# Performance work log

Hardware: AMD Instinct MI355X
Metric: run time of the kernel (lower is better)

The kernel has to match this reference:

```python
import jax, jax.numpy as jnp
import numpy as np

N, N_E, E_DIM = 32768, 4096, 256


def setup_inputs() -> dict:
    key = jax.random.key(0)
    k1, k2 = jax.random.split(key)
    z = jax.random.normal(k1, (N, E_DIM), dtype=jnp.float32)
    # embedding.weight.data.uniform_(-1/n_e, 1/n_e)
    emb = jax.random.uniform(k2, (N_E, E_DIM), dtype=jnp.float32,
                             minval=-1.0 / N_E, maxval=1.0 / N_E)
    return {"z": z, "emb": emb}


def reference(z, emb):
    # pairwise squared L2: ||z||^2 + ||e||^2 - 2 z e^T  -> [N, n_e]
    d = (jnp.sum(z ** 2, axis=1, keepdims=True)
         + jnp.sum(emb ** 2, axis=1)
         - 2.0 * jnp.matmul(z, emb.T))
    min_encoding_indices = jnp.argmin(d, axis=1)              # [N]
    # original builds one-hot scatter and returns it
    min_encodings = jax.nn.one_hot(min_encoding_indices, emb.shape[0],
                                   dtype=z.dtype)             # [N, n_e]
    # one_hot @ emb == direct gather (same math, efficient form)
    z_q = emb[min_encoding_indices]                           # [N, e_dim]
    # loss = mean((z_q - z.detach())^2): codebook loss only (beta unused)
    loss = jnp.mean((z_q - jax.lax.stop_gradient(z)) ** 2)
    # straight-through estimator
    z_q_st = z + jax.lax.stop_gradient(z_q - z)
    return (loss, min_encodings, z_q_st, emb, min_encoding_indices[:, None])
```

## Files before the change

### kernel.cpp

```cpp
#include <hip/hip_runtime.h>
#include <stdint.h>

#define N_ROWS 32768
#define N_E    4096
#define E_DIM  256

typedef __attribute__((ext_vector_type(8))) short short8;
typedef __attribute__((ext_vector_type(4))) float f32x4;

#define GLOAD_LDS16(g, l)                                                     \
    __builtin_amdgcn_global_load_lds(                                         \
        (const __attribute__((address_space(1))) void*)(g),                   \
        (__attribute__((address_space(3))) void*)(l), 16, 0, 0)

__device__ __forceinline__ unsigned int f2sort(float s) {
    unsigned int b = __float_as_uint(s);
    return (b & 0x80000000u) ? ~b : (b | 0x80000000u);
}
__device__ __forceinline__ float sort2f(unsigned int u) {
    unsigned int b = (u & 0x80000000u) ? (u ^ 0x80000000u) : ~u;
    return __uint_as_float(b);
}
__device__ __forceinline__ unsigned short bfr(float x) {
    unsigned int u = __float_as_uint(x);
    return (unsigned short)((u + 0x7fffu + ((u >> 16) & 1u)) >> 16);
}
__device__ __forceinline__ float bf2f(unsigned short h) {
    return __uint_as_float((unsigned int)h << 16);
}

__global__ __launch_bounds__(256) void k_rownorm(const float* __restrict__ src,
                                                 float* __restrict__ outf) {
    int j = blockIdx.x * 4 + (threadIdx.x >> 6);
    int lane = threadIdx.x & 63;
    const float4* e4 = (const float4*)(src + (size_t)j * E_DIM);
    float4 v = e4[lane];
    double s = (double)v.x * v.x + (double)v.y * v.y + (double)v.z * v.z + (double)v.w * v.w;
    #pragma unroll
    for (int off = 1; off < 64; off <<= 1) s += __shfl_xor(s, off);
    if (lane == 0) outf[j] = (float)s;
}

__global__ __launch_bounds__(256) void k_split(const float* __restrict__ src,
                                               unsigned short* __restrict__ hi,
                                               unsigned short* __restrict__ lo) {
    int c = blockIdx.x * 256 + threadIdx.x;
    int r   = c >> 5;
    int kc8 = c & 31;
    const float* p = src + (size_t)c * 8;
    float v[8];
    *(float4*)&v[0] = *(const float4*)p;
    *(float4*)&v[4] = *(const float4*)(p + 4);
    short8 h8, l8;
    #pragma unroll
    for (int t = 0; t < 8; t++) {
        unsigned short h = bfr(v[t]);
        h8[t] = (short)h;
        l8[t] = (short)bfr(v[t] - bf2f(h));
    }
    int kt = kc8 >> 2, lg = kc8 & 3;
    size_t o8 = (size_t)(r >> 4) * 512 + kt * 64 + lg * 16 + (r & 15);
    *(short8*)(hi + o8 * 8) = h8;
    *(short8*)(lo + o8 * 8) = l8;
}

__global__ __launch_bounds__(256, 1) void k_screen(
        const float* __restrict__ z,
        const unsigned short* __restrict__ ehi, const unsigned short* __restrict__ elo,
        const float* __restrict__ enf, const float* __restrict__ znf,
        int* __restrict__ idx, int* __restrict__ flaglist, int* __restrict__ flagcnt,
        float* __restrict__ out) {
    __shared__ short8 BT[8192];

    const int tid  = threadIdx.x;
    const int lane = tid & 63;
    const int w    = tid >> 6;
    const int l15  = lane & 15;
    const int lg   = lane >> 4;
    const int fb0  = blockIdx.x * 8 + w * 2;

    const short8* Gh = (const short8*)ehi;
    const short8* Gl = (const short8*)elo;
    float* zfill = out + (size_t)blockIdx.x * 524288;

    short8 ah[2][8], al[2][8];
    #pragma unroll
    for (int mi = 0; mi < 2; mi++) {
        int row = (fb0 + mi) * 16 + l15;
        const float* zr = z + (size_t)row * E_DIM + lg * 8;
        #pragma unroll
        for (int kt = 0; kt < 8; kt++) {
            float4 v0 = *(const float4*)(zr + kt * 32);
            float4 v1 = *(const float4*)(zr + kt * 32 + 4);
            float v[8] = {v0.x, v0.y, v0.z, v0.w, v1.x, v1.y, v1.z, v1.w};
            short8 h8, l8;
            #pragma unroll
            for (int t = 0; t < 8; t++) {
                unsigned short h = bfr(v[t]);
                h8[t] = (short)h;
                l8[t] = (short)bfr(v[t] - bf2f(h));
            }
            ah[mi][kt] = h8;
            al[mi][kt] = l8;
        }
    }

    float czs[8];
    #pragma unroll
    for (int mi = 0; mi < 2; mi++)
        #pragma unroll
        for (int qi = 0; qi < 4; qi++)
            czs[mi * 4 + qi] = znf[(fb0 + mi) * 16 + lg * 4 + qi];

    unsigned long long K1[8];
    float Qf[8];
    #pragma unroll
    for (int s = 0; s < 8; s++) { K1[s] = ~0ull; Qf[s] = __uint_as_float(0x7F800000u); }

    auto stage = [&](int t, int b) {
        const short8* sh = Gh + (size_t)t * 2048;
        const short8* sl = Gl + (size_t)t * 2048;
        short8* dh = &BT[b * 4096];
        short8* dl = &BT[b * 4096 + 2048];
        #pragma unroll
        for (int i = 0; i < 8; i++) {
            int c = (w * 8 + i) * 64;
            GLOAD_LDS16(sh + c + lane, dh + c);
            GLOAD_LDS16(sl + c + lane, dl + c);
        }
    };

#define LOADB(BH, BL, KT)                                                     \
    _Pragma("unroll")                                                         \
    for (int p = 0; p < 4; p++) {                                             \
        BH[p] = Bc_h[p * 512 + (KT) * 64 + lane];                             \
        BL[p] = Bc_l[p * 512 + (KT) * 64 + lane];                             \
    }
#define DOMFMA(BH, BL, KT)                                                    \
    _Pragma("unroll")                                                         \
    for (int p = 0; p < 4; p++) {                                             \
        _Pragma("unroll")                                                     \
        for (int mi = 0; mi < 2; mi++) {                                      \
            acc[mi][p] = __builtin_amdgcn_mfma_f32_16x16x32_bf16(ah[mi][KT], BH[p], acc[mi][p], 0, 0, 0); \
            acc[mi][p] = __builtin_amdgcn_mfma_f32_16x16x32_bf16(al[mi][KT], BH[p], acc[mi][p], 0, 0, 0); \
            acc[mi][p] = __builtin_amdgcn_mfma_f32_16x16x32_bf16(ah[mi][KT], BL[p], acc[mi][p], 0, 0, 0); \
        }                                                                     \
    }

    int cur = 0;
    stage(0, 0);
    for (int t = 0; t < 64; ++t) {
        __syncthreads();
        if (t + 1 < 64) stage(t + 1, cur ^ 1);

        {
            f32x4 zv4 = {0.f, 0.f, 0.f, 0.f};
            float* dst = zfill + (size_t)t * 8192 + tid * 4;
            #pragma unroll
            for (int i = 0; i < 8; i++)
                __builtin_nontemporal_store(zv4, (f32x4*)(dst + i * 1024));
        }

        const short8* Bc_h = &BT[cur * 4096];
        const short8* Bc_l = &BT[cur * 4096 + 2048];

        f32x4 acc[2][4];
        #pragma unroll
        for (int mi = 0; mi < 2; mi++)
            #pragma unroll
            for (int p = 0; p < 4; p++)
                acc[mi][p] = (f32x4){0.f, 0.f, 0.f, 0.f};

        short8 bhA[4], blA[4], bhB[4], blB[4];
        LOADB(bhA, blA, 0)
        LOADB(bhB, blB, 1)
        DOMFMA(bhA, blA, 0) LOADB(bhA, blA, 2)
        DOMFMA(bhB, blB, 1) LOADB(bhB, blB, 3)
        DOMFMA(bhA, blA, 2) LOADB(bhA, blA, 4)
        DOMFMA(bhB, blB, 3) LOADB(bhB, blB, 5)
        DOMFMA(bhA, blA, 4) LOADB(bhA, blA, 6)
        DOMFMA(bhB, blB, 5) LOADB(bhB, blB, 7)
        DOMFMA(bhA, blA, 6)
        DOMFMA(bhB, blB, 7)

        #pragma unroll
        for (int p = 0; p < 4; p++) {
            int j = t * 64 + p * 16 + l15;
            float Ce = enf[j];
            #pragma unroll
            for (int mi = 0; mi < 2; mi++) {
                #pragma unroll
                for (int qi = 0; qi < 4; qi++) {
                    int s = mi * 4 + qi;
                    float av = acc[mi][p][qi];
                    float A  = czs[s] + Ce;
                    float qv = fmaf(-2.0f, av, A);
                    unsigned long long kk =
                        ((unsigned long long)f2sort(qv) << 32) | (unsigned int)j;
                    if (kk < K1[s]) K1[s] = kk;
                    float res = (A - qv) - 2.0f * av;
                    float u = __uint_as_float(__float_as_uint(qv) & 0x7F800000u)
                              * 1.1920929e-7f;
                    if (fabsf(res) > fmaf(0.5f, u, -1.5e-7f))
                        Qf[s] = fminf(Qf[s], qv);
                }
            }
        }
        cur ^= 1;
    }
#undef LOADB
#undef DOMFMA

    #pragma unroll
    for (int s = 0; s < 8; s++) {
        unsigned long long K = K1[s];
        float Q = Qf[s];
        #pragma unroll
        for (int off = 1; off < 16; off <<= 1) {
            unsigned long long ok = __shfl_xor(K, off);
            float oq = __shfl_xor(Q, off);
            if (ok < K) K = ok;
            Q = fminf(Q, oq);
        }
        if (l15 == 0) {
            int row = blockIdx.x * 128 + w * 32 + (s >> 2) * 16 + lg * 4 + (s & 3);
            idx[row] = (int)(K & 0xFFFFFFFFull);
            float qwin = sort2f((unsigned int)(K >> 32));
            float u = __uint_as_float(__float_as_uint(qwin) & 0x7F800000u) * 1.1920929e-7f;
            if (Q <= fmaf(2.0f, u, qwin)) {
                int pp = atomicAdd(flagcnt, 1);
                flaglist[pp] = row;
            }
        }
    }
}

__global__ __launch_bounds__(256) void k_repair(const float* __restrict__ z,
                                                const float* __restrict__ emb,
                                                const float* __restrict__ enf,
                                                const float* __restrict__ znf,
                                                const int* __restrict__ flagcnt,
                                                const int* __restrict__ flaglist,
                                                unsigned long long* __restrict__ kpart) {
    __shared__ float zr[8][E_DIM];
    __shared__ unsigned long long redk[4][8];
    const int tid = threadIdx.x;
    const int cnt = flagcnt[0];
    const int oct = blockIdx.x >> 2;
    const int qd  = blockIdx.x & 3;

    for (int base = oct * 8; base < cnt; base += 2048) {
        __syncthreads();
        int gr[8];
        #pragma unroll
        for (int r = 0; r < 8; r++) {
            int fi = base + r;
            gr[r] = flaglist[fi < cnt ? fi : base];
        }
        for (int i = tid; i < 8 * 64; i += 256) {
            int r = i >> 6, c4 = i & 63;
            *(float4*)&zr[r][c4 * 4] = *(const float4*)(z + (size_t)gr[r] * E_DIM + c4 * 4);
        }
        __syncthreads();

        float Cz[8];
        #pragma unroll
        for (int r = 0; r < 8; r++) Cz[r] = znf[gr[r]];

        unsigned long long bk[8];
        #pragma unroll
        for (int r = 0; r < 8; r++) bk[r] = ~0ull;

        #pragma unroll
        for (int g = 0; g < 2; g++) {
            const int j0 = qd * 1024 + g * 512 + tid;
            const float* e0 = emb + (size_t)(j0      ) * E_DIM;
            const float* e1 = emb + (size_t)(j0 + 256) * E_DIM;
            float a[8][2];
            #pragma unroll
            for (int r = 0; r < 8; r++) { a[r][0] = 0.0f; a[r][1] = 0.0f; }

            #pragma unroll 4
            for (int k4 = 0; k4 < 64; k4++) {
                float4 v0 = *(const float4*)(e0 + k4 * 4);
                float4 v1 = *(const float4*)(e1 + k4 * 4);
                #pragma unroll
                for (int r = 0; r < 8; r++) {
                    float4 zq = *(const float4*)&zr[r][k4 * 4];
                    a[r][0] = fmaf(zq.x, v0.x, a[r][0]); a[r][0] = fmaf(zq.y, v0.y, a[r][0]);
                    a[r][0] = fmaf(zq.z, v0.z, a[r][0]); a[r][0] = fmaf(zq.w, v0.w, a[r][0]);
                    a[r][1] = fmaf(zq.x, v1.x, a[r][1]); a[r][1] = fmaf(zq.y, v1.y, a[r][1]);
                    a[r][1] = fmaf(zq.z, v1.z, a[r][1]); a[r][1] = fmaf(zq.w, v1.w, a[r][1]);
                }
            }
            float en0 = enf[j0], en1 = enf[j0 + 256];
            #pragma unroll
            for (int r = 0; r < 8; r++) {
                float q0 = (Cz[r] + en0) - 2.0f * a[r][0];
                float q1 = (Cz[r] + en1) - 2.0f * a[r][1];
                unsigned long long k;
                k = ((unsigned long long)f2sort(q0) << 32) | (unsigned int)(j0      ); if (k < bk[r]) bk[r] = k;
                k = ((unsigned long long)f2sort(q1) << 32) | (unsigned int)(j0 + 256); if (k < bk[r]) bk[r] = k;
            }
        }

        const int w = tid >> 6;
        #pragma unroll
        for (int r = 0; r < 8; r++) {
            unsigned long long K = bk[r];
            #pragma unroll
            for (int off = 1; off < 64; off <<= 1) {
                unsigned long long ok = __shfl_xor(K, off);
                if (ok < K) K = ok;
            }
            if ((tid & 63) == 0) redk[w][r] = K;
        }
        __syncthreads();
        if (tid < 8 && base + tid < cnt) {
            unsigned long long K = redk[0][tid];
            #pragma unroll
            for (int wv = 1; wv < 4; wv++)
                if (redk[wv][tid] < K) K = redk[wv][tid];
            kpart[(size_t)(base + tid) * 4 + qd] = K;
        }
    }
}

__global__ __launch_bounds__(256) void k_fin(const int* __restrict__ flagcnt,
                                             const int* __restrict__ flaglist,
                                             const unsigned long long* __restrict__ kpart,
                                             int* __restrict__ idx) {
    const int cnt = flagcnt[0];
    for (int fi = blockIdx.x * 256 + threadIdx.x; fi < cnt; fi += gridDim.x * 256) {
        unsigned long long K = kpart[(size_t)fi * 4];
        #pragma unroll
        for (int qd = 1; qd < 4; qd++) {
            unsigned long long k2 = kpart[(size_t)fi * 4 + qd];
            if (k2 < K) K = k2;
        }
        idx[flaglist[fi]] = (int)(K & 0xFFFFFFFFull);
    }
}

__global__ __launch_bounds__(256) void k_epilogue(const float* __restrict__ z,
                                                  const float* __restrict__ emb,
                                                  const int* __restrict__ idx,
                                                  float* __restrict__ out,
                                                  double* __restrict__ rowloss) {
    const int row  = blockIdx.x * 4 + (threadIdx.x >> 6);
    const int lane = threadIdx.x & 63;
    const int j    = idx[row];
    float4 zv = *(const float4*)(z   + (size_t)row * E_DIM + lane * 4);
    float4 ev = *(const float4*)(emb + (size_t)j   * E_DIM + lane * 4);

    float4 st;
    st.x = zv.x + (ev.x - zv.x);
    st.y = zv.y + (ev.y - zv.y);
    st.z = zv.z + (ev.z - zv.z);
    st.w = zv.w + (ev.w - zv.w);
    const size_t zq0 = 1ull + (size_t)N_ROWS * N_E;
    *(float4*)(out + zq0 + (size_t)row * E_DIM + lane * 4) = st;

    double dx = (double)ev.x - zv.x, dy = (double)ev.y - zv.y;
    double dz = (double)ev.z - zv.z, dw = (double)ev.w - zv.w;
    double s = dx * dx + dy * dy + dz * dz + dw * dw;
    #pragma unroll
    for (int off = 1; off < 64; off <<= 1) s += __shfl_xor(s, off);

    if (lane == 0) {
        rowloss[row] = s;
        if (row == N_ROWS - 1 && j != N_E - 1)
            out[1ull + (size_t)row * N_E + (N_E - 1)] = 0.0f;
        out[1ull + (size_t)row * N_E + j] = 1.0f;
        const size_t ix0 = 1ull + (size_t)N_ROWS * N_E + (size_t)N_ROWS * E_DIM
                         + (size_t)N_E * E_DIM;
        out[ix0 + row] = (float)j;
    }
}

__global__ __launch_bounds__(256) void k_loss(const double* __restrict__ rowloss,
                                              float* __restrict__ out) {
    __shared__ double sm[256];
    double s = 0.0;
    for (int i = threadIdx.x; i < N_ROWS; i += 256) s += rowloss[i];
    sm[threadIdx.x] = s;
    __syncthreads();
    for (int h = 128; h > 0; h >>= 1) {
        if (threadIdx.x < h) sm[threadIdx.x] += sm[threadIdx.x + h];
        __syncthreads();
    }
    if (threadIdx.x == 0)
        out[0] = (float)(sm[0] / ((double)N_ROWS * (double)E_DIM));
}

extern "C" void kernel_launch(void* const* d_in, const int* in_sizes, int n_in,
                              void* d_out, int out_size, void* d_ws, size_t ws_size,
                              hipStream_t stream) {
    const float* z   = (const float*)d_in[0];
    const float* emb = (const float*)d_in[1];
    float* out = (float*)d_out;

    char* ws = (char*)d_ws;
    float*              enf      = (float*)(ws + 0);
    float*              znf      = (float*)(ws + 16384);
    int*                idx      = (int*)(ws + 147456);
    int*                flagcnt  = (int*)(ws + 278528);
    int*                flaglist = (int*)(ws + 278656);
    double*             rowloss  = (double*)(ws + 409728);
    unsigned long long* kpart    = (unsigned long long*)(ws + 671872);
    unsigned short*     ehi      = (unsigned short*)(ws + 1720320);
    unsigned short*     elo      = (unsigned short*)(ws + 3817472);

    hipMemsetAsync(flagcnt, 0, sizeof(int), stream);

    const size_t emb0 = 1ull + (size_t)N_ROWS * N_E + (size_t)N_ROWS * E_DIM;
    hipMemcpyAsync(out + emb0, emb, (size_t)N_E * E_DIM * sizeof(float),
                   hipMemcpyDeviceToDevice, stream);

    k_rownorm <<<N_E / 4, 256, 0, stream>>>(emb, enf);
    k_rownorm <<<N_ROWS / 4, 256, 0, stream>>>(z, znf);
    k_split   <<<N_E / 8, 256, 0, stream>>>(emb, ehi, elo);
    k_screen  <<<256, 256, 0, stream>>>(z, ehi, elo, enf, znf,
                                        idx, flaglist, flagcnt, out);
    k_repair  <<<1024, 256, 0, stream>>>(z, emb, enf, znf, flagcnt, flaglist, kpart);
    k_fin     <<<32, 256, 0, stream>>>(flagcnt, flaglist, kpart, idx);
    k_epilogue<<<N_ROWS / 4, 256, 0, stream>>>(z, emb, idx, out, rowloss);
    k_loss    <<<1, 256, 0, stream>>>(rowloss, out);
}
```

Before: 412.7 us.

## Use two waves per screen block with four row fragments each, loop codebook tiles by column group

```diff
diff --git a/kernel.cpp b/kernel.cpp
--- a/kernel.cpp
+++ b/kernel.cpp
@@ -64,7 +64,7 @@
     *(short8*)(lo + o8 * 8) = l8;
 }
 
-__global__ __launch_bounds__(256, 1) void k_screen(
+__global__ __launch_bounds__(128, 1) void k_screen(
         const float* __restrict__ z,
         const unsigned short* __restrict__ ehi, const unsigned short* __restrict__ elo,
         const float* __restrict__ enf, const float* __restrict__ znf,
@@ -77,15 +77,15 @@
     const int w    = tid >> 6;
     const int l15  = lane & 15;
     const int lg   = lane >> 4;
-    const int fb0  = blockIdx.x * 8 + w * 2;
+    const int fb0  = blockIdx.x * 8 + w * 4;
 
     const short8* Gh = (const short8*)ehi;
     const short8* Gl = (const short8*)elo;
     float* zfill = out + (size_t)blockIdx.x * 524288;
 
-    short8 ah[2][8], al[2][8];
-    #pragma unroll
-    for (int mi = 0; mi < 2; mi++) {
+    short8 ah[4][8], al[4][8];
+    #pragma unroll
+    for (int mi = 0; mi < 4; mi++) {
         int row = (fb0 + mi) * 16 + l15;
         const float* zr = z + (size_t)row * E_DIM + lg * 8;
         #pragma unroll
@@ -105,17 +105,17 @@
         }
     }
 
-    float czs[8];
-    #pragma unroll
-    for (int mi = 0; mi < 2; mi++)
+    float czs[16];
+    #pragma unroll
+    for (int mi = 0; mi < 4; mi++)
         #pragma unroll
         for (int qi = 0; qi < 4; qi++)
             czs[mi * 4 + qi] = znf[(fb0 + mi) * 16 + lg * 4 + qi];
 
-    unsigned long long K1[8];
-    float Qf[8];
-    #pragma unroll
-    for (int s = 0; s < 8; s++) { K1[s] = ~0ull; Qf[s] = __uint_as_float(0x7F800000u); }
+    unsigned long long K1[16];
+    float Qf[16];
+    #pragma unroll
+    for (int s = 0; s < 16; s++) { K1[s] = ~0ull; Qf[s] = __uint_as_float(0x7F800000u); }
 
     auto stage = [&](int t, int b) {
         const short8* sh = Gh + (size_t)t * 2048;
@@ -123,29 +123,12 @@
         short8* dh = &BT[b * 4096];
         short8* dl = &BT[b * 4096 + 2048];
         #pragma unroll
-        for (int i = 0; i < 8; i++) {
-            int c = (w * 8 + i) * 64;
+        for (int i = 0; i < 16; i++) {
+            int c = (w * 16 + i) * 64;
             GLOAD_LDS16(sh + c + lane, dh + c);
             GLOAD_LDS16(sl + c + lane, dl + c);
         }
     };
-
-#define LOADB(BH, BL, KT)                                                     \
-    _Pragma("unroll")                                                         \
-    for (int p = 0; p < 4; p++) {                                             \
-        BH[p] = Bc_h[p * 512 + (KT) * 64 + lane];                             \
-        BL[p] = Bc_l[p * 512 + (KT) * 64 + lane];                             \
-    }
-#define DOMFMA(BH, BL, KT)                                                    \
-    _Pragma("unroll")                                                         \
-    for (int p = 0; p < 4; p++) {                                             \
-        _Pragma("unroll")                                                     \
-        for (int mi = 0; mi < 2; mi++) {                                      \
-            acc[mi][p] = __builtin_amdgcn_mfma_f32_16x16x32_bf16(ah[mi][KT], BH[p], acc[mi][p], 0, 0, 0); \
-            acc[mi][p] = __builtin_amdgcn_mfma_f32_16x16x32_bf16(al[mi][KT], BH[p], acc[mi][p], 0, 0, 0); \
-            acc[mi][p] = __builtin_amdgcn_mfma_f32_16x16x32_bf16(ah[mi][KT], BL[p], acc[mi][p], 0, 0, 0); \
-        }                                                                     \
-    }
 
     int cur = 0;
     stage(0, 0);
@@ -157,42 +140,44 @@
             f32x4 zv4 = {0.f, 0.f, 0.f, 0.f};
             float* dst = zfill + (size_t)t * 8192 + tid * 4;
             #pragma unroll
-            for (int i = 0; i < 8; i++)
-                __builtin_nontemporal_store(zv4, (f32x4*)(dst + i * 1024));
+            for (int i = 0; i < 16; i++)
+                __builtin_nontemporal_store(zv4, (f32x4*)(dst + i * 512));
         }
 
         const short8* Bc_h = &BT[cur * 4096];
         const short8* Bc_l = &BT[cur * 4096 + 2048];
 
-        f32x4 acc[2][4];
-        #pragma unroll
-        for (int mi = 0; mi < 2; mi++)
-            #pragma unroll
-            for (int p = 0; p < 4; p++)
-                acc[mi][p] = (f32x4){0.f, 0.f, 0.f, 0.f};
-
-        short8 bhA[4], blA[4], bhB[4], blB[4];
-        LOADB(bhA, blA, 0)
-        LOADB(bhB, blB, 1)
-        DOMFMA(bhA, blA, 0) LOADB(bhA, blA, 2)
-        DOMFMA(bhB, blB, 1) LOADB(bhB, blB, 3)
-        DOMFMA(bhA, blA, 2) LOADB(bhA, blA, 4)
-        DOMFMA(bhB, blB, 3) LOADB(bhB, blB, 5)
-        DOMFMA(bhA, blA, 4) LOADB(bhA, blA, 6)
-        DOMFMA(bhB, blB, 5) LOADB(bhB, blB, 7)
-        DOMFMA(bhA, blA, 6)
-        DOMFMA(bhB, blB, 7)
-
         #pragma unroll
         for (int p = 0; p < 4; p++) {
+            f32x4 acc[4];
+            #pragma unroll
+            for (int mi = 0; mi < 4; mi++) acc[mi] = (f32x4){0.f, 0.f, 0.f, 0.f};
+
+            short8 bhA = Bc_h[p * 512 + lane], blA = Bc_l[p * 512 + lane];
+            short8 bhB, blB;
+            #pragma unroll
+            for (int kt = 0; kt < 8; kt++) {
+                if (kt < 7) {
+                    bhB = Bc_h[p * 512 + (kt + 1) * 64 + lane];
+                    blB = Bc_l[p * 512 + (kt + 1) * 64 + lane];
+                }
+                #pragma unroll
+                for (int mi = 0; mi < 4; mi++) {
+                    acc[mi] = __builtin_amdgcn_mfma_f32_16x16x32_bf16(ah[mi][kt], bhA, acc[mi], 0, 0, 0);
+                    acc[mi] = __builtin_amdgcn_mfma_f32_16x16x32_bf16(al[mi][kt], bhA, acc[mi], 0, 0, 0);
+                    acc[mi] = __builtin_amdgcn_mfma_f32_16x16x32_bf16(ah[mi][kt], blA, acc[mi], 0, 0, 0);
+                }
+                bhA = bhB; blA = blB;
+            }
+
             int j = t * 64 + p * 16 + l15;
             float Ce = enf[j];
             #pragma unroll
-            for (int mi = 0; mi < 2; mi++) {
+            for (int mi = 0; mi < 4; mi++) {
                 #pragma unroll
                 for (int qi = 0; qi < 4; qi++) {
                     int s = mi * 4 + qi;
-                    float av = acc[mi][p][qi];
+                    float av = acc[mi][qi];
                     float A  = czs[s] + Ce;
                     float qv = fmaf(-2.0f, av, A);
                     unsigned long long kk =
@@ -208,11 +193,9 @@
         }
         cur ^= 1;
     }
-#undef LOADB
-#undef DOMFMA
-
-    #pragma unroll
-    for (int s = 0; s < 8; s++) {
+
+    #pragma unroll
+    for (int s = 0; s < 16; s++) {
         unsigned long long K = K1[s];
         float Q = Qf[s];
         #pragma unroll
@@ -223,7 +206,7 @@
             Q = fminf(Q, oq);
         }
         if (l15 == 0) {
-            int row = blockIdx.x * 128 + w * 32 + (s >> 2) * 16 + lg * 4 + (s & 3);
+            int row = blockIdx.x * 128 + w * 64 + (s >> 2) * 16 + lg * 4 + (s & 3);
             idx[row] = (int)(K & 0xFFFFFFFFull);
             float qwin = sort2f((unsigned int)(K >> 32));
             float u = __uint_as_float(__float_as_uint(qwin) & 0x7F800000u) * 1.1920929e-7f;
@@ -420,7 +403,7 @@
     k_rownorm <<<N_E / 4, 256, 0, stream>>>(emb, enf);
     k_rownorm <<<N_ROWS / 4, 256, 0, stream>>>(z, znf);
     k_split   <<<N_E / 8, 256, 0, stream>>>(emb, ehi, elo);
-    k_screen  <<<256, 256, 0, stream>>>(z, ehi, elo, enf, znf,
+    k_screen  <<<256, 128, 0, stream>>>(z, ehi, elo, enf, znf,
                                         idx, flaglist, flagcnt, out);
     k_repair  <<<1024, 256, 0, stream>>>(z, emb, enf, znf, flagcnt, flaglist, kpart);
     k_fin     <<<32, 256, 0, stream>>>(flagcnt, flaglist, kpart, idx);
```

Result: slower. 727.0 us (+76.2%).
